# Performance work log

Measured on AMD Instinct MI355X. Metric: run time of the kernel, lower is better.

The kernel has to match this reference:

```python
import jax, jax.numpy as jnp
import numpy as np

N, K, D, E, H = 65536, 8, 256, 256, 132  # points, components, latent_dim, encoder_dim, FC hidden

def setup_inputs() -> dict:
    key = jax.random.key(0)
    ks = jax.random.split(key, 12)
    s = 0.05
    f32 = jnp.float32
    return {
        "signal": jax.random.normal(ks[0], (N, E), f32),
        "components": jax.random.normal(ks[1], (K, N, D), f32),
        # message_map / update_map: Linear(D, D)
        "Wm": jax.random.normal(ks[2], (D, D), f32) * s,
        "bm": jnp.zeros((D,), f32),
        "Wu": jax.random.normal(ks[3], (D, D), f32) * s,
        "bu": jnp.zeros((D,), f32),
        "W0": jax.random.normal(ks[4], (H, E + D), f32) * s,
        "b0": jnp.zeros((H,), f32),
        "W1": jax.random.normal(ks[5], (H, H), f32) * s,
        "b1": jnp.zeros((H,), f32),
        "W2": jax.random.normal(ks[6], (H, H), f32) * s,
        "b2": jnpes if False else jnp.zeros((H,), f32),
        "W3": jax.random.normal(ks[7], (D, H), f32) * s,
        "b3": jnp.zeros((D,), f32),
    }

def reference(signal, components, Wm, bm, Wu, bu, W0, b0, W1, b1, W2, b2, W3, b3):
    k = components.shape[0]
    # sum_k Linear(comp_k) == Linear applied to sum, with bias counted k times (linearity)
    right = components.sum(0) @ Wm.T + k * bm          # [N, D]
    right = right @ Wu.T + bu                          # update_map
    x = jnp.concatenate([signal, right], axis=-1)      # [N, E+D]
    x = jax.nn.relu(x @ W0.T + b0)
    x = jax.nn.relu(x @ W1.T + b1)
    x = jax.nn.relu(x @ W2.T + b2)
    return x @ W3.T + b3                               # [N, D]
```

## Files before the change

kernel.cpp:

```cpp
#include <hip/hip_runtime.h>
#include <hip/hip_bf16.h>


typedef float  f32x4  __attribute__((ext_vector_type(4)));
typedef __bf16 bf16x8 __attribute__((ext_vector_type(8)));
typedef unsigned int   u32x2 __attribute__((ext_vector_type(2)));
typedef unsigned short u16x8 __attribute__((ext_vector_type(8)));

__device__ __forceinline__ unsigned short f2bf(float f) {
  unsigned int u = __builtin_bit_cast(unsigned int, f);
  u += 0x7fffu + ((u >> 16) & 1u);
  return (unsigned short)(u >> 16);
}

__device__ __forceinline__ u32x2 pack4(f32x4 v) {
  u32x2 r;
  r[0] = (unsigned)f2bf(v[0]) | ((unsigned)f2bf(v[1]) << 16);
  r[1] = (unsigned)f2bf(v[2]) | ((unsigned)f2bf(v[3]) << 16);
  return r;
}

__device__ __forceinline__ float wave_reduce(float s) {
#pragma unroll
  for (int m = 32; m > 0; m >>= 1) s += __shfl_xor(s, m, 64);
  return s;
}

__global__ __launch_bounds__(256) void kA(const float* __restrict__ comp,
                                          const float* __restrict__ W0,
                                          const float* __restrict__ Wu,
                                          const float* __restrict__ bm,
                                          const float* __restrict__ bu,
                                          float* __restrict__ U,
                                          float* __restrict__ rb,
                                          unsigned short* __restrict__ csum) {
  const int b = blockIdx.x;
  if (b >= 196) {
    const int cb = b - 196;
    const int t = threadIdx.x;
    const f32x4* cp = (const f32x4*)comp;
    const size_t base = (size_t)cb * 2048 + t;
    f32x4 a[8];
#pragma unroll
    for (int j = 0; j < 8; ++j) a[j] = cp[base + j * 256];
#pragma unroll
    for (int k = 1; k < 8; ++k) {
      f32x4 t0[8];
#pragma unroll
      for (int j = 0; j < 8; ++j) t0[j] = cp[base + (size_t)k * 4194304u + j * 256];
#pragma unroll
      for (int j = 0; j < 8; ++j) a[j] += t0[j];
    }
    u32x2* op = (u32x2*)csum;
#pragma unroll
    for (int j = 0; j < 8; ++j) op[base + j * 256] = pack4(a[j]);
  } else if (b < 132) {
    const int h = b, d = threadIdx.x;
    float s = 0.f;
#pragma unroll 8
    for (int i = 0; i < 256; ++i) s += W0[h * 512 + 256 + i] * Wu[i * 256 + d];
    U[h * 256 + d] = s;
  } else {
    const int t = (b - 132) * 4 + (threadIdx.x >> 6);
    const int lane = threadIdx.x & 63;
    f32x4 w = ((const f32x4*)(Wu + t * 256))[lane];
    f32x4 v = ((const f32x4*)bm)[lane];
    float s = w[0] * v[0] + w[1] * v[1] + w[2] * v[2] + w[3] * v[3];
    s = wave_reduce(s);
    if (lane == 0) rb[t] = 8.f * s + bu[t];
  }
}

__global__ __launch_bounds__(256) void kB(const float* __restrict__ U,
                                          const float* __restrict__ Wm,
                                          const float* __restrict__ W0,
                                          const float* __restrict__ rb,
                                          const float* __restrict__ b0,
                                          const float* __restrict__ b1,
                                          const float* __restrict__ b2,
                                          float* __restrict__ Wc,
                                          float* __restrict__ bias1,
                                          float* __restrict__ b1p,
                                          float* __restrict__ b2p) {
  const int b = blockIdx.x;
  if (b < 132) {
    const int h = b, d = threadIdx.x;
    float s = 0.f;
#pragma unroll 8
    for (int j = 0; j < 256; ++j) s += U[h * 256 + j] * Wm[j * 256 + d];
    Wc[h * 256 + d] = s;
  } else {
    const int t = (b - 132) * 4 + (threadIdx.x >> 6);
    const int lane = threadIdx.x & 63;
    float v = 0.f;
    if (t < 132) {
      f32x4 w = ((const f32x4*)(W0 + t * 512 + 256))[lane];
      f32x4 r4 = ((const f32x4*)rb)[lane];
      float s = w[0] * r4[0] + w[1] * r4[1] + w[2] * r4[2] + w[3] * r4[3];
      s = wave_reduce(s);
      v = b0[t] + s;
    }
    if (lane == 0) {
      bias1[t] = v;
      b1p[t] = (t < 132) ? b1[t] : 0.f;
      b2p[t] = (t < 132) ? b2[t] : 0.f;
    }
  }
}

__global__ __launch_bounds__(256) void kC(
    const float* __restrict__ W0, const float* __restrict__ Wc,
    const float* __restrict__ W1, const float* __restrict__ W2,
    const float* __restrict__ W3,
    unsigned short* __restrict__ P1, unsigned short* __restrict__ P2,
    unsigned short* __restrict__ P3, unsigned short* __restrict__ P4) {
  int e = blockIdx.x * 256 + threadIdx.x;
  if (e >= 174080) return;
  unsigned short* dst; int NT, rel, mode;
  if (e < 81920)       { dst = P1; NT = 10; rel = e;          mode = 0; }
  else if (e < 107520) { dst = P2; NT = 10; rel = e - 81920;  mode = 1; }
  else if (e < 133120) { dst = P3; NT = 10; rel = e - 107520; mode = 2; }
  else                 { dst = P4; NT = 16; rel = e - 133120; mode = 3; }
  int chunk = rel >> 9, q = rel & 511;
  int lane = q >> 3, j = q & 7;
  int kk = chunk / NT, nt = chunk - kk * NT;
  int k = kk * 32 + (lane >> 4) * 8 + j;
  int n = nt * 16 + (lane & 15);
  float v = 0.f;
  if (mode == 0) {
    if (n < 132) v = (k < 256) ? W0[n * 512 + k] : Wc[n * 256 + (k - 256)];
  } else if (mode == 1) {
    if (n < 132 && k < 132) v = W1[n * 132 + k];
  } else if (mode == 2) {
    if (n < 132 && k < 132) v = W2[n * 132 + k];
  } else {
    if (k < 132) v = W3[n * 132 + k];
  }
  dst[rel] = f2bf(v);
}

#define WISS(BUF, CHUNK)                                                     \
  {                                                                          \
    _Pragma("unroll") for (int nt = 0; nt < 10; ++nt)                        \
        BUF[nt] = *(const bf16x8*)(Pb + (CHUNK) * 10240 + nt * 1024 +        \
                                   lane * 16);                               \
  }
#define WISS8L4(BUF, Q)                                                      \
  {                                                                          \
    _Pragma("unroll") for (int nt = 0; nt < 8; ++nt)                         \
        BUF[nt] = *(const bf16x8*)(Pb + 266240 + ((Q) % 5) * 16384 +         \
                                   ((Q) / 5) * 8192 + nt * 1024 + lane * 16);\
  }
#define MFMA10(ACC, BUF, AF)                                                 \
  {                                                                          \
    _Pragma("unroll") for (int nt = 0; nt < 10; ++nt)                        \
        ACC[nt] = __builtin_amdgcn_mfma_f32_16x16x32_bf16(AF, BUF[nt],       \
                                                          ACC[nt], 0, 0, 0); \
  }

__global__ __launch_bounds__(256, 2) void kD(
    const float* __restrict__ signal, const unsigned short* __restrict__ csum,
    const unsigned short* __restrict__ Pseq,
    const float* __restrict__ bias1, const float* __restrict__ b1p,
    const float* __restrict__ b2p, const float* __restrict__ b3,
    float* __restrict__ out) {
  extern __shared__ char lds[];
  const int tid = threadIdx.x;
  const int wave = tid >> 6;
  const int lane = tid & 63;
  const int lhalf = lane >> 4;
  const int l16 = lane & 15;
  const int r2 = lane >> 5, c32 = lane & 31;
  char* act0 = lds + wave * 16384;
  char* act1 = act0 + 8192;
  const char* Pb = (const char*)Pseq;
  const int row0 = ((int)blockIdx.x * 4 + wave) * 32;
  const int asw = (l16 & 7) << 4;
  const f32x4* sp = (const f32x4*)signal;

  {
    f32x4 sg[16];
#pragma unroll
    for (int r = 0; r < 16; ++r) sg[r] = sp[(size_t)(row0 + r) * 64 + lane];
#pragma unroll
    for (int r = 0; r < 16; ++r)
      *(u32x2*)(act0 + r * 512 + ((lane * 8) ^ ((r & 7) << 4))) = pack4(sg[r]);
  }
  {
    f32x4 sg[16];
#pragma unroll
    for (int r = 0; r < 16; ++r)
      sg[r] = sp[(size_t)(row0 + 16 + r) * 64 + lane];
#pragma unroll
    for (int r = 0; r < 16; ++r)
      *(u32x2*)(act1 + r * 512 + ((lane * 8) ^ ((r & 7) << 4))) = pack4(sg[r]);
  }

  u16x8 cs0[8], cs1[8];
#pragma unroll
  for (int j = 0; j < 8; ++j)
    cs0[j] = *(const u16x8*)(csum + (size_t)(row0 + 2 * j + r2) * 256 + c32 * 8);
#pragma unroll
  for (int j = 0; j < 8; ++j)
    cs1[j] =
        *(const u16x8*)(csum + (size_t)(row0 + 16 + 2 * j + r2) * 256 + c32 * 8);

  bf16x8 wA[10], wB[10];
  WISS(wA, 0);

  f32x4 acc0[10], acc1[10];
#pragma unroll
  for (int i = 0; i < 10; ++i) {
    acc0[i] = f32x4{0.f, 0.f, 0.f, 0.f};
    acc1[i] = f32x4{0.f, 0.f, 0.f, 0.f};
  }

#pragma unroll
  for (int kk = 0; kk < 8; ++kk) {
    if ((kk + 1) & 1) { WISS(wB, kk + 1); } else { WISS(wA, kk + 1); }
    bf16x8 af0 =
        *(const bf16x8*)(act0 + l16 * 512 + ((kk * 64 + lhalf * 16) ^ asw));
    bf16x8 af1 =
        *(const bf16x8*)(act1 + l16 * 512 + ((kk * 64 + lhalf * 16) ^ asw));
    __builtin_amdgcn_s_setprio(1);
    if (kk & 1) {
      MFMA10(acc0, wB, af0); MFMA10(acc1, wB, af1);
    } else {
      MFMA10(acc0, wA, af0); MFMA10(acc1, wA, af1);
    }
    __builtin_amdgcn_s_setprio(0);
  }

  asm volatile("" ::: "memory");
#pragma unroll
  for (int j = 0; j < 8; ++j) {
    const int rw = 2 * j + r2;
    *(u16x8*)(act0 + rw * 512 + ((c32 * 16) ^ ((rw & 7) << 4))) = cs0[j];
    *(u16x8*)(act1 + rw * 512 + ((c32 * 16) ^ ((rw & 7) << 4))) = cs1[j];
  }
  asm volatile("" ::: "memory");

#pragma unroll
  for (int kk = 8; kk < 16; ++kk) {
    if ((kk + 1) & 1) { WISS(wB, kk + 1); } else { WISS(wA, kk + 1); }
    bf16x8 af0 = *(const bf16x8*)(act0 + l16 * 512 +
                                  (((kk - 8) * 64 + lhalf * 16) ^ asw));
    bf16x8 af1 = *(const bf16x8*)(act1 + l16 * 512 +
                                  (((kk - 8) * 64 + lhalf * 16) ^ asw));
    __builtin_amdgcn_s_setprio(1);
    if (kk & 1) {
      MFMA10(acc0, wB, af0); MFMA10(acc1, wB, af1);
    } else {
      MFMA10(acc0, wA, af0); MFMA10(acc1, wA, af1);
    }
    __builtin_amdgcn_s_setprio(0);
  }

  {
    float bv[10];
#pragma unroll
    for (int nt = 0; nt < 10; ++nt) bv[nt] = bias1[nt * 16 + l16];
    asm volatile("" ::: "memory");
#pragma unroll
    for (int nt = 0; nt < 10; ++nt) {
#pragma unroll
      for (int r = 0; r < 4; ++r) {
        const int row = lhalf * 4 + r;
        const int off = (((nt * 16 + l16) * 2) ^ ((row & 7) << 4));
        float v0 = fmaxf(acc0[nt][r] + bv[nt], 0.f);
        float v1 = fmaxf(acc1[nt][r] + bv[nt], 0.f);
        *(unsigned short*)(act0 + row * 512 + off) = f2bf(v0);
        *(unsigned short*)(act1 + row * 512 + off) = f2bf(v1);
      }
    }
    asm volatile("" ::: "memory");
  }

  bf16x8 w4A[8], w4B[8];
#pragma unroll
  for (int L = 0; L < 2; ++L) {
    const float* hbias = L ? b2p : b1p;
#pragma unroll
    for (int i = 0; i < 10; ++i) {
      acc0[i] = f32x4{0.f, 0.f, 0.f, 0.f};
      acc1[i] = f32x4{0.f, 0.f, 0.f, 0.f};
    }
#pragma unroll
    for (int qq = 0; qq < 5; ++qq) {
      const int cc = 16 + L * 5 + qq;
      if (cc < 25) {
        if (cc & 1) { WISS(wA, cc + 1); } else { WISS(wB, cc + 1); }
      } else {
        WISS8L4(w4A, 0);
      }
      bf16x8 af0 =
          *(const bf16x8*)(act0 + l16 * 512 + ((qq * 64 + lhalf * 16) ^ asw));
      bf16x8 af1 =
          *(const bf16x8*)(act1 + l16 * 512 + ((qq * 64 + lhalf * 16) ^ asw));
      __builtin_amdgcn_s_setprio(1);
      if (cc & 1) {
        MFMA10(acc0, wB, af0); MFMA10(acc1, wB, af1);
      } else {
        MFMA10(acc0, wA, af0); MFMA10(acc1, wA, af1);
      }
      __builtin_amdgcn_s_setprio(0);
    }
    float bv[10];
#pragma unroll
    for (int nt = 0; nt < 10; ++nt) bv[nt] = hbias[nt * 16 + l16];
    asm volatile("" ::: "memory");
#pragma unroll
    for (int nt = 0; nt < 10; ++nt) {
#pragma unroll
      for (int r = 0; r < 4; ++r) {
        const int row = lhalf * 4 + r;
        const int off = (((nt * 16 + l16) * 2) ^ ((row & 7) << 4));
        float v0 = fmaxf(acc0[nt][r] + bv[nt], 0.f);
        float v1 = fmaxf(acc1[nt][r] + bv[nt], 0.f);
        *(unsigned short*)(act0 + row * 512 + off) = f2bf(v0);
        *(unsigned short*)(act1 + row * 512 + off) = f2bf(v1);
      }
    }
    asm volatile("" ::: "memory");
  }

#pragma unroll
  for (int h = 0; h < 2; ++h) {
    f32x4 a40[8], a41[8];
#pragma unroll
    for (int i = 0; i < 8; ++i) {
      a40[i] = f32x4{0.f, 0.f, 0.f, 0.f};
      a41[i] = f32x4{0.f, 0.f, 0.f, 0.f};
    }
#pragma unroll
    for (int kk = 0; kk < 5; ++kk) {
      const int q = h * 5 + kk;
      if (q < 9) {
        if (q & 1) { WISS8L4(w4A, q + 1); } else { WISS8L4(w4B, q + 1); }
      }
      bf16x8 af0 =
          *(const bf16x8*)(act0 + l16 * 512 + ((kk * 64 + lhalf * 16) ^ asw));
      bf16x8 af1 =
          *(const bf16x8*)(act1 + l16 * 512 + ((kk * 64 + lhalf * 16) ^ asw));
      __builtin_amdgcn_s_setprio(1);
#pragma unroll
      for (int i = 0; i < 8; ++i) {
        if (q & 1) {
          a40[i] = __builtin_amdgcn_mfma_f32_16x16x32_bf16(af0, w4B[i], a40[i],
                                                           0, 0, 0);
          a41[i] = __builtin_amdgcn_mfma_f32_16x16x32_bf16(af1, w4B[i], a41[i],
                                                           0, 0, 0);
        } else {
          a40[i] = __builtin_amdgcn_mfma_f32_16x16x32_bf16(af0, w4A[i], a40[i],
                                                           0, 0, 0);
          a41[i] = __builtin_amdgcn_mfma_f32_16x16x32_bf16(af1, w4A[i], a41[i],
                                                           0, 0, 0);
        }
      }
      __builtin_amdgcn_s_setprio(0);
    }
    float bv[8];
#pragma unroll
    for (int i = 0; i < 8; ++i) bv[i] = b3[(h * 8 + i) * 16 + l16];
    float* op0 = out + (size_t)(row0 + lhalf * 4) * 256 + h * 128 + l16;
    float* op1 = out + (size_t)(row0 + 16 + lhalf * 4) * 256 + h * 128 + l16;
#pragma unroll
    for (int i = 0; i < 8; ++i) {
#pragma unroll
      for (int r = 0; r < 4; ++r) {
        op0[(size_t)r * 256 + i * 16] = a40[i][r] + bv[i];
        op1[(size_t)r * 256 + i * 16] = a41[i][r] + bv[i];
      }
    }
  }
}

extern "C" void kernel_launch(void* const* d_in, const int* in_sizes, int n_in,
                              void* d_out, int out_size, void* d_ws, size_t ws_size,
                              hipStream_t stream) {
  const float* signal = (const float*)d_in[0];
  const float* comp   = (const float*)d_in[1];
  const float* Wm = (const float*)d_in[2];
  const float* bm = (const float*)d_in[3];
  const float* Wu = (const float*)d_in[4];
  const float* bu = (const float*)d_in[5];
  const float* W0 = (const float*)d_in[6];
  const float* b0 = (const float*)d_in[7];
  const float* W1 = (const float*)d_in[8];
  const float* b1 = (const float*)d_in[9];
  const float* W2 = (const float*)d_in[10];
  const float* b2 = (const float*)d_in[11];
  const float* W3 = (const float*)d_in[12];
  const float* b3 = (const float*)d_in[13];

  char* ws = (char*)d_ws;
  float* U     = (float*)(ws + 0);
  float* Wc    = (float*)(ws + 135168);
  float* bias1 = (float*)(ws + 270336);
  float* b1p   = (float*)(ws + 270976);
  float* b2p   = (float*)(ws + 271616);
  float* rb    = (float*)(ws + 272256);
  unsigned short* P1 = (unsigned short*)(ws + 273408);
  unsigned short* P2 = (unsigned short*)(ws + 437248);
  unsigned short* P3 = (unsigned short*)(ws + 488448);
  unsigned short* P4 = (unsigned short*)(ws + 539648);
  unsigned short* csum = (unsigned short*)(ws + 621568);

  hipLaunchKernelGGL(kA, dim3(2244), dim3(256), 0, stream,
                     comp, W0, Wu, bm, bu, U, rb, csum);
  hipLaunchKernelGGL(kB, dim3(172), dim3(256), 0, stream,
                     U, Wm, W0, rb, b0, b1, b2, Wc, bias1, b1p, b2p);
  hipLaunchKernelGGL(kC, dim3(680), dim3(256), 0, stream,
                     W0, Wc, W1, W2, W3, P1, P2, P3, P4);
  hipLaunchKernelGGL(kD, dim3(512), dim3(256), 65536, stream,
                     signal, csum, P1, bias1, b1p, b2p, b3, (float*)d_out);
}
```

Before: 180.3 us.

## Merge weight-precompute kernels to cut launches from four to three

Folds the U and Wc weight products into a single block per hidden row, using shared memory for the intermediate row. The bias chain is folded into one block, and packing of W1/W2/W3 moves into the first kernel so only P1 depends on Wc. This removes one kernel launch and its dependency barrier and shrinks the workspace. In exchange, the Wc blocks become serial two-stage dot products and may lengthen the tail of the first kernel.

After: 175.5 us (median of 3 runs). 2.7% less time.

```diff
diff --git a/kernel.cpp b/kernel.cpp
--- a/kernel.cpp
+++ b/kernel.cpp
@@ -20,26 +20,22 @@
   return r;
 }
 
-__device__ __forceinline__ float wave_reduce(float s) {
-#pragma unroll
-  for (int m = 32; m > 0; m >>= 1) s += __shfl_xor(s, m, 64);
-  return s;
-}
-
-__global__ __launch_bounds__(256) void kA(const float* __restrict__ comp,
-                                          const float* __restrict__ W0,
-                                          const float* __restrict__ Wu,
-                                          const float* __restrict__ bm,
-                                          const float* __restrict__ bu,
-                                          float* __restrict__ U,
-                                          float* __restrict__ rb,
-                                          unsigned short* __restrict__ csum) {
+__global__ __launch_bounds__(256) void kA(
+    const float* __restrict__ comp, const float* __restrict__ W0,
+    const float* __restrict__ Wu, const float* __restrict__ Wm,
+    const float* __restrict__ bm, const float* __restrict__ bu,
+    const float* __restrict__ b0, const float* __restrict__ b1,
+    const float* __restrict__ b2, const float* __restrict__ W1,
+    const float* __restrict__ W2, const float* __restrict__ W3,
+    float* __restrict__ Wc, float* __restrict__ bias1,
+    float* __restrict__ b1p, float* __restrict__ b2p,
+    unsigned short* __restrict__ csum, unsigned short* __restrict__ P2,
+    unsigned short* __restrict__ P3, unsigned short* __restrict__ P4) {
   const int b = blockIdx.x;
-  if (b >= 196) {
-    const int cb = b - 196;
-    const int t = threadIdx.x;
+  const int d = threadIdx.x;
+  if (b < 2048) {
     const f32x4* cp = (const f32x4*)comp;
-    const size_t base = (size_t)cb * 2048 + t;
+    const size_t base = (size_t)b * 2048 + d;
     f32x4 a[8];
 #pragma unroll
     for (int j = 0; j < 8; ++j) a[j] = cp[base + j * 256];
@@ -47,96 +43,90 @@
     for (int k = 1; k < 8; ++k) {
       f32x4 t0[8];
 #pragma unroll
-      for (int j = 0; j < 8; ++j) t0[j] = cp[base + (size_t)k * 4194304u + j * 256];
+      for (int j = 0; j < 8; ++j)
+        t0[j] = cp[base + (size_t)k * 4194304u + j * 256];
 #pragma unroll
       for (int j = 0; j < 8; ++j) a[j] += t0[j];
     }
     u32x2* op = (u32x2*)csum;
 #pragma unroll
     for (int j = 0; j < 8; ++j) op[base + j * 256] = pack4(a[j]);
-  } else if (b < 132) {
-    const int h = b, d = threadIdx.x;
+  } else if (b < 2180) {
+    __shared__ float u[256];
+    const int h = b - 2048;
     float s = 0.f;
 #pragma unroll 8
     for (int i = 0; i < 256; ++i) s += W0[h * 512 + 256 + i] * Wu[i * 256 + d];
-    U[h * 256 + d] = s;
+    u[d] = s;
+    __syncthreads();
+    float s2 = 0.f;
+#pragma unroll 8
+    for (int j = 0; j < 256; ++j) s2 += u[j] * Wm[j * 256 + d];
+    Wc[h * 256 + d] = s2;
+  } else if (b == 2180) {
+    __shared__ float bml[256];
+    __shared__ float rbl[256];
+    bml[d] = bm[d];
+    __syncthreads();
+    {
+      const f32x4* wr = (const f32x4*)(Wu + d * 256);
+      const f32x4* bm4 = (const f32x4*)bml;
+      float s = 0.f;
+#pragma unroll 8
+      for (int i = 0; i < 64; ++i) {
+        f32x4 w = wr[i], v = bm4[i];
+        s += w[0] * v[0] + w[1] * v[1] + w[2] * v[2] + w[3] * v[3];
+      }
+      rbl[d] = 8.f * s + bu[d];
+    }
+    __syncthreads();
+    if (d < 160) {
+      float v = 0.f;
+      if (d < 132) {
+        float s = 0.f;
+#pragma unroll 8
+        for (int j = 0; j < 256; ++j) s += W0[d * 512 + 256 + j] * rbl[j];
+        v = b0[d] + s;
+      }
+      bias1[d] = v;
+      b1p[d] = (d < 132) ? b1[d] : 0.f;
+      b2p[d] = (d < 132) ? b2[d] : 0.f;
+    }
   } else {
-    const int t = (b - 132) * 4 + (threadIdx.x >> 6);
-    const int lane = threadIdx.x & 63;
-    f32x4 w = ((const f32x4*)(Wu + t * 256))[lane];
-    f32x4 v = ((const f32x4*)bm)[lane];
-    float s = w[0] * v[0] + w[1] * v[1] + w[2] * v[2] + w[3] * v[3];
-    s = wave_reduce(s);
-    if (lane == 0) rb[t] = 8.f * s + bu[t];
-  }
-}
-
-__global__ __launch_bounds__(256) void kB(const float* __restrict__ U,
-                                          const float* __restrict__ Wm,
-                                          const float* __restrict__ W0,
-                                          const float* __restrict__ rb,
-                                          const float* __restrict__ b0,
-                                          const float* __restrict__ b1,
-                                          const float* __restrict__ b2,
-                                          float* __restrict__ Wc,
-                                          float* __restrict__ bias1,
-                                          float* __restrict__ b1p,
-                                          float* __restrict__ b2p) {
-  const int b = blockIdx.x;
-  if (b < 132) {
-    const int h = b, d = threadIdx.x;
-    float s = 0.f;
-#pragma unroll 8
-    for (int j = 0; j < 256; ++j) s += U[h * 256 + j] * Wm[j * 256 + d];
-    Wc[h * 256 + d] = s;
-  } else {
-    const int t = (b - 132) * 4 + (threadIdx.x >> 6);
-    const int lane = threadIdx.x & 63;
+    const int e2 = (b - 2181) * 256 + d;
+    unsigned short* dst; int NT, rel, mode;
+    if (e2 < 25600)      { dst = P2; NT = 10; rel = e2;          mode = 1; }
+    else if (e2 < 51200) { dst = P3; NT = 10; rel = e2 - 25600;  mode = 2; }
+    else                 { dst = P4; NT = 16; rel = e2 - 51200;  mode = 3; }
+    int chunk = rel >> 9, q = rel & 511;
+    int lane = q >> 3, j = q & 7;
+    int kk = chunk / NT, nt = chunk - kk * NT;
+    int k = kk * 32 + (lane >> 4) * 8 + j;
+    int n = nt * 16 + (lane & 15);
     float v = 0.f;
-    if (t < 132) {
-      f32x4 w = ((const f32x4*)(W0 + t * 512 + 256))[lane];
-      f32x4 r4 = ((const f32x4*)rb)[lane];
-      float s = w[0] * r4[0] + w[1] * r4[1] + w[2] * r4[2] + w[3] * r4[3];
-      s = wave_reduce(s);
-      v = b0[t] + s;
-    }
-    if (lane == 0) {
-      bias1[t] = v;
-      b1p[t] = (t < 132) ? b1[t] : 0.f;
-      b2p[t] = (t < 132) ? b2[t] : 0.f;
-    }
+    if (mode == 1) {
+      if (n < 132 && k < 132) v = W1[n * 132 + k];
+    } else if (mode == 2) {
+      if (n < 132 && k < 132) v = W2[n * 132 + k];
+    } else {
+      if (k < 132) v = W3[n * 132 + k];
+    }
+    dst[rel] = f2bf(v);
   }
 }
 
 __global__ __launch_bounds__(256) void kC(
     const float* __restrict__ W0, const float* __restrict__ Wc,
-    const float* __restrict__ W1, const float* __restrict__ W2,
-    const float* __restrict__ W3,
-    unsigned short* __restrict__ P1, unsigned short* __restrict__ P2,
-    unsigned short* __restrict__ P3, unsigned short* __restrict__ P4) {
+    unsigned short* __restrict__ P1) {
   int e = blockIdx.x * 256 + threadIdx.x;
-  if (e >= 174080) return;
-  unsigned short* dst; int NT, rel, mode;
-  if (e < 81920)       { dst = P1; NT = 10; rel = e;          mode = 0; }
-  else if (e < 107520) { dst = P2; NT = 10; rel = e - 81920;  mode = 1; }
-  else if (e < 133120) { dst = P3; NT = 10; rel = e - 107520; mode = 2; }
-  else                 { dst = P4; NT = 16; rel = e - 133120; mode = 3; }
-  int chunk = rel >> 9, q = rel & 511;
+  int chunk = e >> 9, q = e & 511;
   int lane = q >> 3, j = q & 7;
-  int kk = chunk / NT, nt = chunk - kk * NT;
+  int kk = chunk / 10, nt = chunk - kk * 10;
   int k = kk * 32 + (lane >> 4) * 8 + j;
   int n = nt * 16 + (lane & 15);
   float v = 0.f;
-  if (mode == 0) {
-    if (n < 132) v = (k < 256) ? W0[n * 512 + k] : Wc[n * 256 + (k - 256)];
-  } else if (mode == 1) {
-    if (n < 132 && k < 132) v = W1[n * 132 + k];
-  } else if (mode == 2) {
-    if (n < 132 && k < 132) v = W2[n * 132 + k];
-  } else {
-    if (k < 132) v = W3[n * 132 + k];
-  }
-  dst[rel] = f2bf(v);
+  if (n < 132) v = (k < 256) ? W0[n * 512 + k] : Wc[n * 256 + (k - 256)];
+  P1[e] = f2bf(v);
 }
 
 #define WISS(BUF, CHUNK)                                                     \
@@ -394,24 +384,20 @@
   const float* b3 = (const float*)d_in[13];
 
   char* ws = (char*)d_ws;
-  float* U     = (float*)(ws + 0);
-  float* Wc    = (float*)(ws + 135168);
-  float* bias1 = (float*)(ws + 270336);
-  float* b1p   = (float*)(ws + 270976);
-  float* b2p   = (float*)(ws + 271616);
-  float* rb    = (float*)(ws + 272256);
-  unsigned short* P1 = (unsigned short*)(ws + 273408);
-  unsigned short* P2 = (unsigned short*)(ws + 437248);
-  unsigned short* P3 = (unsigned short*)(ws + 488448);
-  unsigned short* P4 = (unsigned short*)(ws + 539648);
-  unsigned short* csum = (unsigned short*)(ws + 621568);
-
-  hipLaunchKernelGGL(kA, dim3(2244), dim3(256), 0, stream,
-                     comp, W0, Wu, bm, bu, U, rb, csum);
-  hipLaunchKernelGGL(kB, dim3(172), dim3(256), 0, stream,
-                     U, Wm, W0, rb, b0, b1, b2, Wc, bias1, b1p, b2p);
-  hipLaunchKernelGGL(kC, dim3(680), dim3(256), 0, stream,
-                     W0, Wc, W1, W2, W3, P1, P2, P3, P4);
+  float* Wc    = (float*)(ws + 0);
+  float* bias1 = (float*)(ws + 135168);
+  float* b1p   = (float*)(ws + 135808);
+  float* b2p   = (float*)(ws + 136448);
+  unsigned short* P1 = (unsigned short*)(ws + 137216);
+  unsigned short* P2 = (unsigned short*)(ws + 301056);
+  unsigned short* P3 = (unsigned short*)(ws + 352256);
+  unsigned short* P4 = (unsigned short*)(ws + 403456);
+  unsigned short* csum = (unsigned short*)(ws + 485376);
+
+  hipLaunchKernelGGL(kA, dim3(2541), dim3(256), 0, stream,
+                     comp, W0, Wu, Wm, bm, bu, b0, b1, b2, W1, W2, W3,
+                     Wc, bias1, b1p, b2p, csum, P2, P3, P4);
+  hipLaunchKernelGGL(kC, dim3(320), dim3(256), 0, stream, W0, Wc, P1);
   hipLaunchKernelGGL(kD, dim3(512), dim3(256), 65536, stream,
                      signal, csum, P1, bias1, b1p, b2p, b3, (float*)d_out);
 }
```
